# Kernel optimization log

Measured on AMD Instinct MI355X. Metric: run time of the kernel, lower is better.

## Reference

```python
import jax, jax.numpy as jnp
import numpy as np

D = 256
H = 8
HD = D // H
LN_EPS = 1e-5


def setup_inputs() -> dict:
    key = jax.random.key(0)
    ks = jax.random.split(key, 20)
    N = 768
    s = lambda *sh: 1.0 / np.sqrt(sh[-1])
    inp = {
        "features": jax.random.normal(ks[0], (N, D), jnp.float32),
        "boxes": jax.random.uniform(ks[1], (N, 4), jnp.float32),
        # MultiheadAttention params (torch layout: [out, in])
        "in_proj_w": jax.random.normal(ks[2], (3 * D, D), jnp.float32) * s(D),
        "in_proj_b": jnp.zeros((3 * D,), jnp.float32),
        "out_proj_w": jax.random.normal(ks[3], (D, D), jnp.float32) * s(D),
        "out_proj_b": jnp.zeros((D,), jnp.float32),
        # similarity_net params
        "w1": jax.random.normal(ks[4], (256, 3 * D + 3), jnp.float32) * s(3 * D + 3),
        "b1": jnp.zeros((256,), jnp.float32),
        "ln_g": jnp.ones((256,), jnp.float32),
        "ln_b": jnp.zeros((256,), jnp.float32),
        "w2": jax.random.normal(ks[5], (128, 256), jnp.float32) * s(256),
        "b2": jnp.zeros((128,), jnp.float32),
        "w3": jax.random.normal(ks[6], (64, 128), jnp.float32) * s(128),
        "b3": jnp.zeros((64,), jnp.float32),
        "w4": jax.random.normal(ks[7], (32, 64), jnp.float32) * s(64),
        "b4": jnp.zeros((32,), jnp.float32),
        "w5": jax.random.normal(ks[8], (1, 32), jnp.float32) * s(32),
        "b5": jnp.zeros((1,), jnp.float32),
    }
    return inp


def _mha(x, in_w, in_b, out_w, out_b):
    # x: [N, D]; torch nn.MultiheadAttention self-attention (eval mode)
    N = x.shape[0]
    qkv = x @ in_w.T + in_b                      # [N, 3D]
    q, k, v = jnp.split(qkv, 3, axis=-1)
    q = q.reshape(N, H, HD).transpose(1, 0, 2)   # [H, N, HD]
    k = k.reshape(N, H, HD).transpose(1, 0, 2)
    v = v.reshape(N, H, HD).transpose(1, 0, 2)
    scores = jnp.einsum("hnd,hmd->hnm", q, k) / np.sqrt(HD)
    attn = jax.nn.softmax(scores, axis=-1)
    o = jnp.einsum("hnm,hmd->hnd", attn, v)      # [H, N, HD]
    o = o.transpose(1, 0, 2).reshape(N, D)
    return o @ out_w.T + out_b


def reference(features, boxes, in_proj_w, in_proj_b, out_proj_w, out_proj_b,
              w1, b1, ln_g, ln_b, w2, b2, w3, b3, w4, b4, w5, b5):
    N = features.shape[0]
    att = _mha(features, in_proj_w, in_proj_b, out_proj_w, out_proj_b)  # [N, D]

    fi = jnp.broadcast_to(att[:, None, :], (N, N, D))
    fj = jnp.broadcast_to(att[None, :, :], (N, N, D))
    bi = boxes[:, None, :]
    bj = boxes[None, :, :]
    x_dist = jnp.abs(bi[:, :, 0] - bj[:, :, 0])
    y_diff = bi[:, :, 1] - bj[:, :, 1]
    spatial = jnp.stack([x_dist, jnp.abs(y_diff), y_diff], axis=-1)    # [N, N, 3]
    pairs = jnp.concatenate([fi, fj, fi * fj, spatial], axis=-1)       # [N, N, 3D+3]

    h = jax.nn.relu(pairs @ w1.T + b1)
    mu = jnp.mean(h, axis=-1, keepdims=True)
    var = jnp.var(h, axis=-1, keepdims=True)
    h = (h - mu) / jnp.sqrt(var + LN_EPS) * ln_g + ln_b
    h = jax.nn.relu(h @ w2.T + b2)
    h = jax.nn.relu(h @ w3.T + b3)
    h = jax.nn.relu(h @ w4.T + b4)
    logits = (h @ w5.T + b5)[..., 0]                                   # [N, N]

    eye = jnp.eye(N, dtype=logits.dtype)
    return logits * (1.0 - eye) - 1e9 * eye
```

## Files before the change

### kernel.cpp

```cpp
#include <hip/hip_runtime.h>


typedef __attribute__((ext_vector_type(8))) __bf16 bf16x8;
typedef __attribute__((ext_vector_type(4))) float f32x4;
typedef __attribute__((ext_vector_type(8))) int i32x8;

__device__ __forceinline__ float bf2f(unsigned short u) {
    return __uint_as_float(((unsigned int)u) << 16);
}
__device__ __forceinline__ unsigned short f2bf(float f) {
    union { __bf16 b; unsigned short u; } cv;
    cv.b = (__bf16)f;
    return cv.u;
}
__device__ __forceinline__ unsigned pk2(float lo, float hi) {
    return (unsigned)f2bf(lo) | ((unsigned)f2bf(hi) << 16);
}
__device__ __forceinline__ int pk4_fp8(float a, float b, float c, float d) {
    int w = __builtin_amdgcn_cvt_pk_fp8_f32(a, b, 0, false);
    w = __builtin_amdgcn_cvt_pk_fp8_f32(c, d, w, true);
    return w;
}
__device__ __forceinline__ unsigned char f2fp8(float v) {
    return (unsigned char)(__builtin_amdgcn_cvt_pk_fp8_f32(v, 0.f, 0, false) & 0xff);
}
__device__ __forceinline__ bf16x8 load8f_bf(const float* p) {
    float4 a = *reinterpret_cast<const float4*>(p);
    float4 b = *reinterpret_cast<const float4*>(p + 4);
    union { bf16x8 v; unsigned u[4]; } cv;
    cv.u[0] = pk2(a.x, a.y); cv.u[1] = pk2(a.z, a.w);
    cv.u[2] = pk2(b.x, b.y); cv.u[3] = pk2(b.z, b.w);
    return cv.v;
}
__device__ __forceinline__ i32x8 ld32_lds(const unsigned char* p) {
    union { i32x8 v; uint4 q[2]; } r;
    r.q[0] = *reinterpret_cast<const uint4*>(p);
    r.q[1] = *reinterpret_cast<const uint4*>(p + 16);
    return r.v;
}
#define SC1 0x7F7F7F7F
#define MFMA_MX(a, b, c) __builtin_amdgcn_mfma_scale_f32_16x16x128_f8f6f4( \
        (a), (b), (c), 0, 0, 0, SC1, 0, SC1)

__global__ __launch_bounds__(256) void pack_all(
    const float* __restrict__ features, const float* __restrict__ in_proj_w,
    const float* __restrict__ in_proj_b, const float* __restrict__ out_proj_w,
    const float* __restrict__ w1, const float* __restrict__ w2,
    const float* __restrict__ w3, const float* __restrict__ w4,
    const float* __restrict__ b1, const float* __restrict__ ln_g,
    const float* __restrict__ ln_b, const float* __restrict__ b2,
    const float* __restrict__ out_proj_b,
    unsigned short* __restrict__ qkvb, unsigned short* __restrict__ Vt,
    unsigned short* __restrict__ WcatB,
    unsigned char* __restrict__ w1c_mx, unsigned char* __restrict__ w1t_f8,
    unsigned char* __restrict__ w2g_mx, unsigned char* __restrict__ w3_mx,
    unsigned char* __restrict__ w4_f8,
    float* __restrict__ bias768, float* __restrict__ c1, float* __restrict__ c2)
{
    const int blk = blockIdx.x;
    if (blk < 716) {
        int t = blk * 256 + threadIdx.x;
        if (t < 65536) {
            WcatB[t] = f2bf(out_proj_w[t]);
        } else if (t < 131072) {
            int u = t - 65536;
            int e = u & 31, lane = (u >> 5) & 63, f = u >> 11;
            int mt = f & 15, ks = f >> 4;
            int o = mt * 16 + (lane & 15);
            int k = ks * 128 + ((lane >> 4) & 3) * 32 + e;
            w1c_mx[u] = f2fp8(w1[o * 771 + 512 + k]);
        } else if (t < 139264) {
            int u = t - 131072;
            int e = u & 7, lane = (u >> 3) & 63, f = u >> 9;
            int o = f * 16 + (lane & 15);
            int k = ((lane >> 4) & 3) * 8 + e;
            float v = (k < 3) ? w1[o * 771 + 768 + k] : 0.f;
            w1t_f8[u] = f2fp8(v);
        } else if (t < 172032) {
            int u = t - 139264;
            int e = u & 31, lane = (u >> 5) & 63, f = u >> 11;
            int mt = f & 7, ks = f >> 3;
            int p = mt * 16 + (lane & 15);
            int k = ks * 128 + ((lane >> 4) & 3) * 32 + e;
            w2g_mx[u] = f2fp8(w2[p * 256 + k] * ln_g[k]);
        } else if (t < 180224) {
            int u = t - 172032;
            int e = u & 31, lane = (u >> 5) & 63, f = u >> 11;
            int o = f * 16 + (lane & 15);
            int k = ((lane >> 4) & 3) * 32 + e;
            w3_mx[u] = f2fp8(w3[o * 128 + k]);
        } else if (t < 182272) {
            int u = t - 180224;
            int e = u & 7, lane = (u >> 3) & 63, f = u >> 9;
            int l15 = lane & 15, quad = lane >> 4;
            int ct = f & 1, kc = f >> 1;
            int o = ct * 16 + l15, k = kc * 32 + quad * 8 + e;
            w4_f8[u] = f2fp8(w4[o * 64 + k]);
        } else if (t < 183040) {
            int n = t - 182272;
            if (n < 256) bias768[n] = out_proj_b[n];
            else {
                int m = n - 256;
                float s = 0.f;
                for (int d = 0; d < 256; d += 4) {
                    float4 ob = *reinterpret_cast<const float4*>(&out_proj_b[d]);
                    const float* wr = (m < 256) ? &w1[m * 771 + d]
                                                : &w1[(m - 256) * 771 + 256 + d];
                    float4 w = *reinterpret_cast<const float4*>(wr);
                    s += ob.x * w.x + ob.y * w.y + ob.z * w.z + ob.w * w.w;
                }
                bias768[n] = s + ((m < 256) ? b1[m] : 0.f);
            }
        } else if (t < 183168) {
            int p = t - 183040;
            float s2 = 0.f, s1 = 0.f;
            for (int k = 0; k < 256; k += 4) {
                float4 w = *reinterpret_cast<const float4*>(&w2[p * 256 + k]);
                float4 g = *reinterpret_cast<const float4*>(&ln_g[k]);
                float4 lb = *reinterpret_cast<const float4*>(&ln_b[k]);
                s2 += g.x * w.x + g.y * w.y + g.z * w.z + g.w * w.w;
                s1 += lb.x * w.x + lb.y * w.y + lb.z * w.z + lb.w * w.w;
            }
            c2[p] = s2;
            c1[p] = s1 + b2[p];
        }
    } else if (blk < 1228) {
        const int n = blk - 716, e = threadIdx.x;
        const float* wrow = (n < 256) ? &w1[n * 771] : &w1[(n - 256) * 771 + 256];
        float acc = 0.f;
        for (int d = 0; d < 256; d += 4) {
            float4 w = *reinterpret_cast<const float4*>(&wrow[d]);
            acc += w.x * out_proj_w[(d + 0) * 256 + e];
            acc += w.y * out_proj_w[(d + 1) * 256 + e];
            acc += w.z * out_proj_w[(d + 2) * 256 + e];
            acc += w.w * out_proj_w[(d + 3) * 256 + e];
        }
        WcatB[(256 + n) * 256 + e] = f2bf(acc);
    } else {
        const int q = blk - 1228;
        const int bm = q % 12, bn = q / 12;
        const int wv = threadIdx.x >> 6, lane = threadIdx.x & 63;
        const int l15 = lane & 15, quad = lane >> 4;
        const int row0 = bm * 64 + wv * 16;
        const int col0 = bn * 64;
        f32x4 acc[4] = {};
        for (int kc = 0; kc < 8; ++kc) {
            bf16x8 a = load8f_bf(&features[(row0 + l15) * 256 + kc * 32 + quad * 8]);
#pragma unroll
            for (int ct = 0; ct < 4; ++ct) {
                bf16x8 b = load8f_bf(&in_proj_w[(col0 + ct * 16 + l15) * 256 + kc * 32 + quad * 8]);
                acc[ct] = __builtin_amdgcn_mfma_f32_16x16x32_bf16(a, b, acc[ct], 0, 0, 0);
            }
        }
#pragma unroll
        for (int ct = 0; ct < 4; ++ct)
#pragma unroll
            for (int r = 0; r < 4; ++r) {
                int row = row0 + quad * 4 + r, col = col0 + ct * 16 + l15;
                float v = acc[ct][r] + in_proj_b[col];
                if (col < 512) qkvb[row * 768 + col] = f2bf(v);
                else           Vt[(col - 512) * 768 + row] = f2bf(v);
            }
    }
}

__global__ __launch_bounds__(256) void gemm_attab(
    const unsigned short* __restrict__ A, const unsigned short* __restrict__ W,
    const float* __restrict__ bias, float* __restrict__ att,
    float* __restrict__ AB)
{
    const int wv = threadIdx.x >> 6, lane = threadIdx.x & 63;
    const int l15 = lane & 15, quad = lane >> 4;
    const int row0 = blockIdx.x * 64 + wv * 16;
    const int col0 = blockIdx.y * 64;
    f32x4 acc[4] = {};
    for (int kc = 0; kc < 8; ++kc) {
        bf16x8 a = *reinterpret_cast<const bf16x8*>(&A[(row0 + l15) * 256 + kc * 32 + quad * 8]);
#pragma unroll
        for (int ct = 0; ct < 4; ++ct) {
            bf16x8 b = *reinterpret_cast<const bf16x8*>(&W[(col0 + ct * 16 + l15) * 256 + kc * 32 + quad * 8]);
            acc[ct] = __builtin_amdgcn_mfma_f32_16x16x32_bf16(a, b, acc[ct], 0, 0, 0);
        }
    }
#pragma unroll
    for (int ct = 0; ct < 4; ++ct)
#pragma unroll
        for (int r = 0; r < 4; ++r) {
            int row = row0 + quad * 4 + r, col = col0 + ct * 16 + l15;
            float v = acc[ct][r] + bias[col];
            if (col < 256) att[row * 256 + col] = v;
            else           AB[row * 512 + (col - 256)] = v;
        }
}

#define SP 776

__global__ __launch_bounds__(256) void attn_mfma(
    const unsigned short* __restrict__ qkvb, const unsigned short* __restrict__ Vt,
    unsigned short* __restrict__ Obf)
{
    __shared__ __align__(16) unsigned short smS[32 * SP];
    __shared__ float s_inv[32];
    const int h = blockIdx.x, q0 = blockIdx.y * 32, hb = h * 32;
    const int tid = threadIdx.x, wave = tid >> 6, lane = tid & 63;
    const int l15 = lane & 15, quad = lane >> 4;

    bf16x8 af[2];
#pragma unroll
    for (int mt = 0; mt < 2; ++mt)
        af[mt] = *reinterpret_cast<const bf16x8*>(&qkvb[(q0 + mt * 16 + l15) * 768 + hb + quad * 8]);
#pragma unroll
    for (int ct = 0; ct < 12; ++ct) {
        int n0 = wave * 192 + ct * 16;
        bf16x8 b = *reinterpret_cast<const bf16x8*>(&qkvb[(n0 + l15) * 768 + 256 + hb + quad * 8]);
#pragma unroll
        for (int mt = 0; mt < 2; ++mt) {
            f32x4 c = {};
            c = __builtin_amdgcn_mfma_f32_16x16x32_bf16(af[mt], b, c, 0, 0, 0);
#pragma unroll
            for (int r = 0; r < 4; ++r)
                smS[(mt * 16 + quad * 4 + r) * SP + n0 + l15] =
                    f2bf(c[r] * 0.17677669529663689f);
        }
    }
    __syncthreads();

    {
        const int row = tid >> 3, part = tid & 7;
        unsigned short* rp = &smS[row * SP + part * 96];
        float ls = 0.f;
#pragma unroll
        for (int c8 = 0; c8 < 12; ++c8) {
            uint4 v = *reinterpret_cast<const uint4*>(&rp[c8 * 8]);
            const unsigned short* pe = reinterpret_cast<const unsigned short*>(&v);
            unsigned short o8[8];
#pragma unroll
            for (int e = 0; e < 8; ++e) {
                float ev = __expf(bf2f(pe[e]));
                ls += ev;
                o8[e] = f2bf(ev);
            }
            *reinterpret_cast<uint4*>(&rp[c8 * 8]) = *reinterpret_cast<const uint4*>(o8);
        }
        ls += __shfl_xor(ls, 1, 64);
        ls += __shfl_xor(ls, 2, 64);
        ls += __shfl_xor(ls, 4, 64);
        if (part == 0) s_inv[row] = 1.0f / ls;
    }
    __syncthreads();

    const int row0 = (wave >> 1) * 16, cg = wave & 1;
    f32x4 accp = {};
    for (int kc = 0; kc < 24; ++kc) {
        bf16x8 a = *reinterpret_cast<const bf16x8*>(&smS[(row0 + l15) * SP + kc * 32 + quad * 8]);
        bf16x8 b = *reinterpret_cast<const bf16x8*>(&Vt[(hb + cg * 16 + l15) * 768 + kc * 32 + quad * 8]);
        accp = __builtin_amdgcn_mfma_f32_16x16x32_bf16(a, b, accp, 0, 0, 0);
    }
#pragma unroll
    for (int r = 0; r < 4; ++r) {
        int rloc = row0 + quad * 4 + r;
        Obf[(q0 + rloc) * 256 + hb + cg * 16 + l15] = f2bf(accp[r] * s_inv[rloc]);
    }
}

#define S1 304
#define S2 144
#define S3 72

__global__ __launch_bounds__(512, 2) void pair_mlp(
    const float* __restrict__ att, const float* __restrict__ AB,
    const unsigned char* __restrict__ w1c_mx, const unsigned char* __restrict__ w1t_f8,
    const unsigned char* __restrict__ w2g_mx, const unsigned char* __restrict__ w3_mx,
    const unsigned char* __restrict__ w4_f8,
    const float* __restrict__ boxes,
    const float* __restrict__ c1, const float* __restrict__ c2,
    const float* __restrict__ b3, const float* __restrict__ b4,
    const float* __restrict__ w5, const float* __restrict__ b5,
    float* __restrict__ out)
{
    __shared__ __align__(16) unsigned char smH[64 * S1];
    __shared__ __align__(16) unsigned char smH2[64 * S2];
    __shared__ __align__(16) unsigned char smH3[64 * S3];
    __shared__ float s_psum[64][8], s_pssq[64][8];
    __shared__ float s_mu[64], s_rs[64];
    __shared__ float s_l5[64][2];

    const int i    = blockIdx.x;
    const int j0   = blockIdx.y * 64;
    const int tid  = threadIdx.x;
    const int wave = tid >> 6;
    const int lane = tid & 63;
    const int l15  = lane & 15;
    const int quad = lane >> 4;

    {
        const int g = tid & 63;
        float4 fi4 = *reinterpret_cast<const float4*>(&att[i * 256 + g * 4]);
#pragma unroll 4
        for (int it = 0; it < 8; ++it) {
            int r = (tid >> 6) + it * 8;
            float4 aj = *reinterpret_cast<const float4*>(&att[(j0 + r) * 256 + g * 4]);
            *reinterpret_cast<int*>(&smH[r * S1 + g * 4]) =
                pk4_fp8(aj.x * fi4.x, aj.y * fi4.y, aj.z * fi4.z, aj.w * fi4.w);
        }
    }
    if (tid < 64) {
        int j = j0 + tid;
        float xd = fabsf(boxes[i * 4 + 0] - boxes[j * 4 + 0]);
        float yd = boxes[i * 4 + 1] - boxes[j * 4 + 1];
        *reinterpret_cast<int*>(&smH[tid * S1 + 256]) = pk4_fp8(xd, fabsf(yd), yd, 0.f);
        *reinterpret_cast<int*>(&smH[tid * S1 + 260]) = 0;
        *reinterpret_cast<long long*>(&smH[tid * S1 + 264]) = 0;
        *reinterpret_cast<long long*>(&smH[tid * S1 + 272]) = 0;
        *reinterpret_cast<long long*>(&smH[tid * S1 + 280]) = 0;
    }
    __syncthreads();

    f32x4 acc1[2][4] = {};
#pragma unroll
    for (int ks = 0; ks < 2; ++ks) {
        i32x8 a0 = *reinterpret_cast<const i32x8*>(&w1c_mx[((ks * 16 + wave * 2 + 0) * 64 + lane) * 32]);
        i32x8 a1 = *reinterpret_cast<const i32x8*>(&w1c_mx[((ks * 16 + wave * 2 + 1) * 64 + lane) * 32]);
#pragma unroll
        for (int nt = 0; nt < 4; ++nt) {
            i32x8 b = ld32_lds(&smH[(nt * 16 + l15) * S1 + ks * 128 + quad * 32]);
            acc1[0][nt] = MFMA_MX(a0, b, acc1[0][nt]);
            acc1[1][nt] = MFMA_MX(a1, b, acc1[1][nt]);
        }
    }
    {
        long long a0 = *reinterpret_cast<const long long*>(&w1t_f8[((wave * 2 + 0) * 64 + lane) * 8]);
        long long a1 = *reinterpret_cast<const long long*>(&w1t_f8[((wave * 2 + 1) * 64 + lane) * 8]);
#pragma unroll
        for (int nt = 0; nt < 4; ++nt) {
            long long b = *reinterpret_cast<const long long*>(&smH[(nt * 16 + l15) * S1 + 256 + quad * 8]);
            acc1[0][nt] = __builtin_amdgcn_mfma_f32_16x16x32_fp8_fp8(a0, b, acc1[0][nt], 0, 0, 0);
            acc1[1][nt] = __builtin_amdgcn_mfma_f32_16x16x32_fp8_fp8(a1, b, acc1[1][nt], 0, 0, 0);
        }
    }

    const int o0 = wave * 32;
    float vsum[4] = {}, vssq[4] = {};
#pragma unroll
    for (int mt = 0; mt < 2; ++mt) {
        int o = o0 + mt * 16 + quad * 4;
        float4 Ai = *reinterpret_cast<const float4*>(&AB[i * 512 + o]);
        float AiA[4] = {Ai.x, Ai.y, Ai.z, Ai.w};
#pragma unroll
        for (int nt = 0; nt < 4; ++nt) {
            int j = nt * 16 + l15;
            float4 Bj = *reinterpret_cast<const float4*>(&AB[(j0 + j) * 512 + 256 + o]);
            float BjA[4] = {Bj.x, Bj.y, Bj.z, Bj.w};
#pragma unroll
            for (int r = 0; r < 4; ++r) {
                float v = fmaxf(acc1[mt][nt][r] + AiA[r] + BjA[r], 0.f);
                acc1[mt][nt][r] = v;
                vsum[nt] += v; vssq[nt] += v * v;
            }
        }
    }
#pragma unroll
    for (int nt = 0; nt < 4; ++nt) {
        vsum[nt] += __shfl_xor(vsum[nt], 16, 64);
        vsum[nt] += __shfl_xor(vsum[nt], 32, 64);
        vssq[nt] += __shfl_xor(vssq[nt], 16, 64);
        vssq[nt] += __shfl_xor(vssq[nt], 32, 64);
    }
    if (quad == 0)
#pragma unroll
        for (int nt = 0; nt < 4; ++nt) {
            s_psum[nt * 16 + l15][wave] = vsum[nt];
            s_pssq[nt * 16 + l15][wave] = vssq[nt];
        }
    __syncthreads();
#pragma unroll
    for (int mt = 0; mt < 2; ++mt) {
        int o = o0 + mt * 16 + quad * 4;
#pragma unroll
        for (int nt = 0; nt < 4; ++nt) {
            int j = nt * 16 + l15;
            *reinterpret_cast<int*>(&smH[j * S1 + o]) =
                pk4_fp8(acc1[mt][nt][0], acc1[mt][nt][1], acc1[mt][nt][2], acc1[mt][nt][3]);
        }
    }
    if (wave == 0) {
        int j = lane;
        float sm = 0.f, sq = 0.f;
#pragma unroll
        for (int w = 0; w < 8; ++w) { sm += s_psum[j][w]; sq += s_pssq[j][w]; }
        sm *= (1.0f / 256.0f); sq *= (1.0f / 256.0f);
        s_mu[j] = sm;
        s_rs[j] = rsqrtf(sq - sm * sm + 1e-5f);
    }
    __syncthreads();

    f32x4 acc2[4] = {};
#pragma unroll
    for (int ks = 0; ks < 2; ++ks) {
        i32x8 a = *reinterpret_cast<const i32x8*>(&w2g_mx[((ks * 8 + wave) * 64 + lane) * 32]);
#pragma unroll
        for (int nt = 0; nt < 4; ++nt) {
            i32x8 b = ld32_lds(&smH[(nt * 16 + l15) * S1 + ks * 128 + quad * 32]);
            acc2[nt] = MFMA_MX(a, b, acc2[nt]);
        }
    }
    {
        int p = wave * 16 + quad * 4;
        float4 C1 = *reinterpret_cast<const float4*>(&c1[p]);
        float4 C2 = *reinterpret_cast<const float4*>(&c2[p]);
        float C1A[4] = {C1.x, C1.y, C1.z, C1.w};
        float C2A[4] = {C2.x, C2.y, C2.z, C2.w};
#pragma unroll
        for (int nt = 0; nt < 4; ++nt) {
            int j = nt * 16 + l15;
            float mu = s_mu[j], rs = s_rs[j];
            float vv[4];
#pragma unroll
            for (int r = 0; r < 4; ++r)
                vv[r] = fmaxf(rs * (acc2[nt][r] - mu * C2A[r]) + C1A[r], 0.f);
            *reinterpret_cast<int*>(&smH2[j * S2 + p]) = pk4_fp8(vv[0], vv[1], vv[2], vv[3]);
        }
    }
    __syncthreads();

    const int qt  = wave >> 1;
    const int jh2 = wave & 1;
    f32x4 acc3[2] = {};
    {
        i32x8 a = *reinterpret_cast<const i32x8*>(&w3_mx[(qt * 64 + lane) * 32]);
#pragma unroll
        for (int ntl = 0; ntl < 2; ++ntl) {
            int j = (jh2 * 2 + ntl) * 16 + l15;
            i32x8 b = ld32_lds(&smH2[j * S2 + quad * 32]);
            acc3[ntl] = MFMA_MX(a, b, acc3[ntl]);
        }
    }
    {
        int q = qt * 16 + quad * 4;
        float4 B3 = *reinterpret_cast<const float4*>(&b3[q]);
        float B3A[4] = {B3.x, B3.y, B3.z, B3.w};
#pragma unroll
        for (int ntl = 0; ntl < 2; ++ntl) {
            int j = (jh2 * 2 + ntl) * 16 + l15;
            float vv[4];
#pragma unroll
            for (int r = 0; r < 4; ++r)
                vv[r] = fmaxf(acc3[ntl][r] + B3A[r], 0.f);
            *reinterpret_cast<int*>(&smH3[j * S3 + q]) = pk4_fp8(vv[0], vv[1], vv[2], vv[3]);
        }
    }
    __syncthreads();

    const int mt4 = wave & 1;
    const int jq  = wave >> 1;
    f32x4 acc4 = {};
#pragma unroll
    for (int kc = 0; kc < 2; ++kc) {
        long long a = *reinterpret_cast<const long long*>(&w4_f8[((kc * 2 + mt4) * 64 + lane) * 8]);
        int j = jq * 16 + l15;
        long long b = *reinterpret_cast<const long long*>(&smH3[j * S3 + kc * 32 + quad * 8]);
        acc4 = __builtin_amdgcn_mfma_f32_16x16x32_fp8_fp8(a, b, acc4, 0, 0, 0);
    }
    {
        int o4 = mt4 * 16 + quad * 4;
        float4 B4 = *reinterpret_cast<const float4*>(&b4[o4]);
        float4 W5 = *reinterpret_cast<const float4*>(&w5[o4]);
        float B4A[4] = {B4.x, B4.y, B4.z, B4.w};
        float W5A[4] = {W5.x, W5.y, W5.z, W5.w};
        float part = 0.f;
#pragma unroll
        for (int r = 0; r < 4; ++r)
            part += fmaxf(acc4[r] + B4A[r], 0.f) * W5A[r];
        part += __shfl_xor(part, 16, 64);
        part += __shfl_xor(part, 32, 64);
        if (quad == 0)
            s_l5[jq * 16 + l15][mt4] = part;
    }
    __syncthreads();
    if (tid < 64) {
        int j = j0 + tid;
        float v = s_l5[tid][0] + s_l5[tid][1] + b5[0];
        out[i * 768 + j] = (j == i) ? -1.0e9f : v;
    }
}

extern "C" void kernel_launch(void* const* d_in, const int* in_sizes, int n_in,
                              void* d_out, int out_size, void* d_ws, size_t ws_size,
                              hipStream_t stream)
{
    const float* features   = (const float*)d_in[0];
    const float* boxes      = (const float*)d_in[1];
    const float* in_proj_w  = (const float*)d_in[2];
    const float* in_proj_b  = (const float*)d_in[3];
    const float* out_proj_w = (const float*)d_in[4];
    const float* out_proj_b = (const float*)d_in[5];
    const float* w1  = (const float*)d_in[6];
    const float* b1  = (const float*)d_in[7];
    const float* ln_g = (const float*)d_in[8];
    const float* ln_b = (const float*)d_in[9];
    const float* w2  = (const float*)d_in[10];
    const float* b2  = (const float*)d_in[11];
    const float* w3  = (const float*)d_in[12];
    const float* b3  = (const float*)d_in[13];
    const float* w4  = (const float*)d_in[14];
    const float* b4  = (const float*)d_in[15];
    const float* w5  = (const float*)d_in[16];
    const float* b5  = (const float*)d_in[17];
    float* out = (float*)d_out;

    char* p = (char*)d_ws;
    unsigned short* qkvb  = (unsigned short*)p; p += 768 * 768 * 2;
    unsigned short* Vt    = (unsigned short*)p; p += 256 * 768 * 2;
    unsigned short* Obf   = (unsigned short*)p; p += 768 * 256 * 2;
    unsigned short* WcatB = (unsigned short*)p; p += 196608 * 2;
    float* att = (float*)p; p += 768 * 256 * 4;
    float* AB  = (float*)p; p += 768 * 512 * 4;
    unsigned char* w1c_mx = (unsigned char*)p; p += 65536;
    unsigned char* w1t_f8 = (unsigned char*)p; p += 8192;
    unsigned char* w2g_mx = (unsigned char*)p; p += 32768;
    unsigned char* w3_mx  = (unsigned char*)p; p += 8192;
    unsigned char* w4_f8  = (unsigned char*)p; p += 2048;
    float* bias768 = (float*)p; p += 768 * 4;
    float* c1v     = (float*)p; p += 128 * 4;
    float* c2v     = (float*)p; p += 128 * 4;

    pack_all<<<dim3(1372), dim3(256), 0, stream>>>(features, in_proj_w,
        in_proj_b, out_proj_w, w1, w2, w3, w4, b1, ln_g, ln_b, b2, out_proj_b,
        qkvb, Vt, WcatB, w1c_mx, w1t_f8, w2g_mx, w3_mx, w4_f8,
        bias768, c1v, c2v);
    attn_mfma<<<dim3(8, 24), dim3(256), 0, stream>>>(qkvb, Vt, Obf);
    gemm_attab<<<dim3(12, 12), dim3(256), 0, stream>>>(Obf, WcatB, bias768,
        att, AB);
    pair_mlp<<<dim3(768, 12), dim3(512), 0, stream>>>(att, AB,
        w1c_mx, w1t_f8, w2g_mx, w3_mx, w4_f8, boxes, c1v, c2v,
        b3, b4, w5, b5, out);
}
```

Before: 297.0 us.

## XOR-swizzle pair_mlp LDS buffers and split layer-1 output into separate buffer

Replaces the padded-stride LDS layouts in pair_mlp with XOR-swizzled 16-byte chunk layouts for the layer-1 input, layer-1 output and layer-2 output, so the 32-byte MFMA operand reads avoid bank conflicts. Layer-1 results now go to a new smH1 buffer rather than overwriting smH, which removes one barrier before the writeback and moves another. LDS use per block grows substantially, which may reduce how many blocks fit per CU under launch_bounds(512,2).

```diff
diff --git a/kernel.cpp b/kernel.cpp
--- a/kernel.cpp
+++ b/kernel.cpp
@@ -31,12 +31,6 @@
     cv.u[0] = pk2(a.x, a.y); cv.u[1] = pk2(a.z, a.w);
     cv.u[2] = pk2(b.x, b.y); cv.u[3] = pk2(b.z, b.w);
     return cv.v;
-}
-__device__ __forceinline__ i32x8 ld32_lds(const unsigned char* p) {
-    union { i32x8 v; uint4 q[2]; } r;
-    r.q[0] = *reinterpret_cast<const uint4*>(p);
-    r.q[1] = *reinterpret_cast<const uint4*>(p + 16);
-    return r.v;
 }
 #define SC1 0x7F7F7F7F
 #define MFMA_MX(a, b, c) __builtin_amdgcn_mfma_scale_f32_16x16x128_f8f6f4( \
@@ -263,10 +257,6 @@
     }
 }
 
-#define S1 304
-#define S2 144
-#define S3 72
-
 __global__ __launch_bounds__(512, 2) void pair_mlp(
     const float* __restrict__ att, const float* __restrict__ AB,
     const unsigned char* __restrict__ w1c_mx, const unsigned char* __restrict__ w1t_f8,
@@ -278,9 +268,10 @@
     const float* __restrict__ w5, const float* __restrict__ b5,
     float* __restrict__ out)
 {
-    __shared__ __align__(16) unsigned char smH[64 * S1];
-    __shared__ __align__(16) unsigned char smH2[64 * S2];
-    __shared__ __align__(16) unsigned char smH3[64 * S3];
+    __shared__ __align__(16) unsigned char smH[64 * 384];
+    __shared__ __align__(16) unsigned char smH1[64 * 256];
+    __shared__ __align__(16) unsigned char smH2[64 * 192];
+    __shared__ __align__(16) unsigned char smH3[64 * 72];
     __shared__ float s_psum[64][8], s_pssq[64][8];
     __shared__ float s_mu[64], s_rs[64];
     __shared__ float s_l5[64][2];
@@ -295,12 +286,14 @@
 
     {
         const int g = tid & 63;
+        const int ch = g >> 2;
         float4 fi4 = *reinterpret_cast<const float4*>(&att[i * 256 + g * 4]);
 #pragma unroll 4
         for (int it = 0; it < 8; ++it) {
             int r = (tid >> 6) + it * 8;
             float4 aj = *reinterpret_cast<const float4*>(&att[(j0 + r) * 256 + g * 4]);
-            *reinterpret_cast<int*>(&smH[r * S1 + g * 4]) =
+            int cs = ch ^ (r & 15);
+            *reinterpret_cast<int*>(&smH[r * 384 + cs * 16 + (g & 3) * 4]) =
                 pk4_fp8(aj.x * fi4.x, aj.y * fi4.y, aj.z * fi4.z, aj.w * fi4.w);
         }
     }
@@ -308,11 +301,12 @@
         int j = j0 + tid;
         float xd = fabsf(boxes[i * 4 + 0] - boxes[j * 4 + 0]);
         float yd = boxes[i * 4 + 1] - boxes[j * 4 + 1];
-        *reinterpret_cast<int*>(&smH[tid * S1 + 256]) = pk4_fp8(xd, fabsf(yd), yd, 0.f);
-        *reinterpret_cast<int*>(&smH[tid * S1 + 260]) = 0;
-        *reinterpret_cast<long long*>(&smH[tid * S1 + 264]) = 0;
-        *reinterpret_cast<long long*>(&smH[tid * S1 + 272]) = 0;
-        *reinterpret_cast<long long*>(&smH[tid * S1 + 280]) = 0;
+        unsigned char* tb = &smH[tid * 384 + 256 + (tid & 3) * 24];
+        *reinterpret_cast<int*>(tb)      = pk4_fp8(xd, fabsf(yd), yd, 0.f);
+        *reinterpret_cast<int*>(tb + 4)  = 0;
+        *reinterpret_cast<long long*>(tb + 8)  = 0;
+        *reinterpret_cast<long long*>(tb + 16) = 0;
+        *reinterpret_cast<long long*>(tb + 24) = 0;
     }
     __syncthreads();
 
@@ -321,11 +315,15 @@
     for (int ks = 0; ks < 2; ++ks) {
         i32x8 a0 = *reinterpret_cast<const i32x8*>(&w1c_mx[((ks * 16 + wave * 2 + 0) * 64 + lane) * 32]);
         i32x8 a1 = *reinterpret_cast<const i32x8*>(&w1c_mx[((ks * 16 + wave * 2 + 1) * 64 + lane) * 32]);
-#pragma unroll
-        for (int nt = 0; nt < 4; ++nt) {
-            i32x8 b = ld32_lds(&smH[(nt * 16 + l15) * S1 + ks * 128 + quad * 32]);
-            acc1[0][nt] = MFMA_MX(a0, b, acc1[0][nt]);
-            acc1[1][nt] = MFMA_MX(a1, b, acc1[1][nt]);
+        const int cb = ks * 8 + quad * 2;
+#pragma unroll
+        for (int nt = 0; nt < 4; ++nt) {
+            const unsigned char* rp = &smH[(nt * 16 + l15) * 384];
+            union { i32x8 v; uint4 q[2]; } b;
+            b.q[0] = *reinterpret_cast<const uint4*>(rp + ((cb    ) ^ l15) * 16);
+            b.q[1] = *reinterpret_cast<const uint4*>(rp + ((cb + 1) ^ l15) * 16);
+            acc1[0][nt] = MFMA_MX(a0, b.v, acc1[0][nt]);
+            acc1[1][nt] = MFMA_MX(a1, b.v, acc1[1][nt]);
         }
     }
     {
@@ -333,7 +331,8 @@
         long long a1 = *reinterpret_cast<const long long*>(&w1t_f8[((wave * 2 + 1) * 64 + lane) * 8]);
 #pragma unroll
         for (int nt = 0; nt < 4; ++nt) {
-            long long b = *reinterpret_cast<const long long*>(&smH[(nt * 16 + l15) * S1 + 256 + quad * 8]);
+            long long b = *reinterpret_cast<const long long*>(
+                &smH[(nt * 16 + l15) * 384 + 256 + (l15 & 3) * 24 + quad * 8]);
             acc1[0][nt] = __builtin_amdgcn_mfma_f32_16x16x32_fp8_fp8(a0, b, acc1[0][nt], 0, 0, 0);
             acc1[1][nt] = __builtin_amdgcn_mfma_f32_16x16x32_fp8_fp8(a1, b, acc1[1][nt], 0, 0, 0);
         }
@@ -372,17 +371,17 @@
             s_psum[nt * 16 + l15][wave] = vsum[nt];
             s_pssq[nt * 16 + l15][wave] = vssq[nt];
         }
-    __syncthreads();
 #pragma unroll
     for (int mt = 0; mt < 2; ++mt) {
-        int o = o0 + mt * 16 + quad * 4;
+        const int ch = wave * 2 + mt;
 #pragma unroll
         for (int nt = 0; nt < 4; ++nt) {
             int j = nt * 16 + l15;
-            *reinterpret_cast<int*>(&smH[j * S1 + o]) =
+            *reinterpret_cast<int*>(&smH1[j * 256 + (ch ^ l15) * 16 + quad * 4]) =
                 pk4_fp8(acc1[mt][nt][0], acc1[mt][nt][1], acc1[mt][nt][2], acc1[mt][nt][3]);
         }
     }
+    __syncthreads();
     if (wave == 0) {
         int j = lane;
         float sm = 0.f, sq = 0.f;
@@ -392,18 +391,22 @@
         s_mu[j] = sm;
         s_rs[j] = rsqrtf(sq - sm * sm + 1e-5f);
     }
-    __syncthreads();
 
     f32x4 acc2[4] = {};
 #pragma unroll
     for (int ks = 0; ks < 2; ++ks) {
         i32x8 a = *reinterpret_cast<const i32x8*>(&w2g_mx[((ks * 8 + wave) * 64 + lane) * 32]);
-#pragma unroll
-        for (int nt = 0; nt < 4; ++nt) {
-            i32x8 b = ld32_lds(&smH[(nt * 16 + l15) * S1 + ks * 128 + quad * 32]);
-            acc2[nt] = MFMA_MX(a, b, acc2[nt]);
-        }
-    }
+        const int cb = ks * 8 + quad * 2;
+#pragma unroll
+        for (int nt = 0; nt < 4; ++nt) {
+            const unsigned char* rp = &smH1[(nt * 16 + l15) * 256];
+            union { i32x8 v; uint4 q[2]; } b;
+            b.q[0] = *reinterpret_cast<const uint4*>(rp + ((cb    ) ^ l15) * 16);
+            b.q[1] = *reinterpret_cast<const uint4*>(rp + ((cb + 1) ^ l15) * 16);
+            acc2[nt] = MFMA_MX(a, b.v, acc2[nt]);
+        }
+    }
+    __syncthreads();
     {
         int p = wave * 16 + quad * 4;
         float4 C1 = *reinterpret_cast<const float4*>(&c1[p]);
@@ -418,7 +421,8 @@
 #pragma unroll
             for (int r = 0; r < 4; ++r)
                 vv[r] = fmaxf(rs * (acc2[nt][r] - mu * C2A[r]) + C1A[r], 0.f);
-            *reinterpret_cast<int*>(&smH2[j * S2 + p]) = pk4_fp8(vv[0], vv[1], vv[2], vv[3]);
+            *reinterpret_cast<int*>(&smH2[j * 192 + (wave ^ (l15 & 7)) * 16 + quad * 4]) =
+                pk4_fp8(vv[0], vv[1], vv[2], vv[3]);
         }
     }
     __syncthreads();
@@ -428,11 +432,15 @@
     f32x4 acc3[2] = {};
     {
         i32x8 a = *reinterpret_cast<const i32x8*>(&w3_mx[(qt * 64 + lane) * 32]);
+        const int cb = quad * 2;
 #pragma unroll
         for (int ntl = 0; ntl < 2; ++ntl) {
             int j = (jh2 * 2 + ntl) * 16 + l15;
-            i32x8 b = ld32_lds(&smH2[j * S2 + quad * 32]);
-            acc3[ntl] = MFMA_MX(a, b, acc3[ntl]);
+            const unsigned char* rp = &smH2[j * 192];
+            union { i32x8 v; uint4 q[2]; } b;
+            b.q[0] = *reinterpret_cast<const uint4*>(rp + ((cb    ) ^ (l15 & 7)) * 16);
+            b.q[1] = *reinterpret_cast<const uint4*>(rp + ((cb + 1) ^ (l15 & 7)) * 16);
+            acc3[ntl] = MFMA_MX(a, b.v, acc3[ntl]);
         }
     }
     {
@@ -446,7 +454,7 @@
 #pragma unroll
             for (int r = 0; r < 4; ++r)
                 vv[r] = fmaxf(acc3[ntl][r] + B3A[r], 0.f);
-            *reinterpret_cast<int*>(&smH3[j * S3 + q]) = pk4_fp8(vv[0], vv[1], vv[2], vv[3]);
+            *reinterpret_cast<int*>(&smH3[j * 72 + q]) = pk4_fp8(vv[0], vv[1], vv[2], vv[3]);
         }
     }
     __syncthreads();
@@ -458,7 +466,7 @@
     for (int kc = 0; kc < 2; ++kc) {
         long long a = *reinterpret_cast<const long long*>(&w4_f8[((kc * 2 + mt4) * 64 + lane) * 8]);
         int j = jq * 16 + l15;
-        long long b = *reinterpret_cast<const long long*>(&smH3[j * S3 + kc * 32 + quad * 8]);
+        long long b = *reinterpret_cast<const long long*>(&smH3[j * 72 + kc * 32 + quad * 8]);
         acc4 = __builtin_amdgcn_mfma_f32_16x16x32_fp8_fp8(a, b, acc4, 0, 0, 0);
     }
     {
```

After: 283.3 us. -4.6%, faster.
